# Optimization experiments

Measured on AMD Instinct MI355X. Metric: run time of the kernel, lower is better.

Reference implementation:

```python
import jax, jax.numpy as jnp
import numpy as np

B, S, I, C, N = 8, 50, 20, 64, 4096  # batch, max seq len, items per set, channels, num_items


def setup_inputs() -> dict:
    key = jax.random.key(0)
    k1, k2, k3, k4, k5 = jax.random.split(key, 5)
    input_tensor = jax.random.normal(k1, (B, S, I, C), dtype=jnp.float32)
    items_id = jax.random.randint(k2, (B, S, I), 0, N)
    # seq lengths in [1, S] (original truncates each user's sequence)
    batch_seq_length = jax.random.randint(k3, (B,), 1, S + 1)
    items_embedding = jax.random.normal(k4, (N, C), dtype=jnp.float32) * 0.02
    proj_w = jax.random.normal(k5, (C, C), dtype=jnp.float32) / jnp.sqrt(jnp.float32(C))
    proj_b = jnp.zeros((C,), dtype=jnp.float32)
    return {
        "input_tensor": input_tensor,
        "items_embedding": items_embedding,
        "proj_w": proj_w,
        "proj_b": proj_b,
        "items_id": items_id,
        "batch_seq_length": batch_seq_length,
    }


def reference(input_tensor, items_embedding, proj_w, proj_b, items_id, batch_seq_length):
    # Dropout layers are identity in eval mode.
    Bb, Ss, Ii, Cc = input_tensor.shape
    Nn = items_embedding.shape[0]

    # valid sequence positions per user: seq_index < batch_seq_length[b]
    seq_mask = (jnp.arange(Ss)[None, :] < batch_seq_length[:, None]).astype(input_tensor.dtype)  # [B,S]
    m = seq_mask[:, :, None]  # [B,S,1], all I item slots valid inside a valid position

    # segment-mean over item occurrences (replaces the Python dict-of-lists + stack/mean)
    flat_ids = (items_id + jnp.arange(Bb)[:, None, None] * Nn).reshape(-1)  # [B*S*I]
    data = (input_tensor * m[..., None]).reshape(-1, Cc)                    # [B*S*I, C]
    sums = jax.ops.segment_sum(data, flat_ids, num_segments=Bb * Nn).reshape(Bb, Nn, Cc)
    counts = jax.ops.segment_sum(jnp.broadcast_to(m, (Bb, Ss, Ii)).reshape(-1),
                                 flat_ids, num_segments=Bb * Nn).reshape(Bb, Nn)
    present = counts > 0                                                    # user's unique historical items
    mean = sums / jnp.maximum(counts, 1.0)[..., None]                       # [B,N,C]

    # attention of all items over the user's unique historical-item embeddings
    scores = jnp.einsum('nc,bmc->bnm', items_embedding, mean)               # [B,N,N]
    scores = jax.nn.leaky_relu(scores, negative_slope=0.2)
    scores = jnp.where(present[:, None, :], scores, jnp.float32(-1e30))     # softmax only over present items
    attn = jax.nn.softmax(scores, axis=-1)
    user_items_embedding = jnp.einsum('bnm,bmc->bnc', attn, mean)           # [B,N,C]

    proj = user_items_embedding @ proj_w.T + proj_b                         # Linear(C,C)
    return (proj * items_embedding[None]).sum(axis=-1)                      # [B,N]
```

## Files before the change

### kernel.cpp

```cpp
#include <hip/hip_runtime.h>

#define Bb 8
#define Ss 50
#define Ii 20
#define Cc 64
#define Nn 4096
#define MAXM 1024
#define POSB (Ss * Ii)

typedef unsigned short ushort_t;
typedef __attribute__((ext_vector_type(8))) short short8;
typedef __attribute__((ext_vector_type(4))) float f32x4;

__device__ inline ushort_t bf16_rn(float x) {
    unsigned u = __float_as_uint(x);
    u = u + 0x7FFFu + ((u >> 16) & 1u);
    return (ushort_t)(u >> 16);
}
__device__ inline float bf16_f(ushort_t h) { return __uint_as_float(((unsigned)h) << 16); }

__device__ inline short8 cvthi8(float4 a, float4 b) {
    short8 r;
    r[0] = (short)bf16_rn(a.x); r[1] = (short)bf16_rn(a.y);
    r[2] = (short)bf16_rn(a.z); r[3] = (short)bf16_rn(a.w);
    r[4] = (short)bf16_rn(b.x); r[5] = (short)bf16_rn(b.y);
    r[6] = (short)bf16_rn(b.z); r[7] = (short)bf16_rn(b.w);
    return r;
}
__device__ inline short8 cvtlo8(float4 a, float4 b, short8 hi) {
    short8 r;
    r[0] = (short)bf16_rn(a.x - bf16_f((ushort_t)hi[0]));
    r[1] = (short)bf16_rn(a.y - bf16_f((ushort_t)hi[1]));
    r[2] = (short)bf16_rn(a.z - bf16_f((ushort_t)hi[2]));
    r[3] = (short)bf16_rn(a.w - bf16_f((ushort_t)hi[3]));
    r[4] = (short)bf16_rn(b.x - bf16_f((ushort_t)hi[4]));
    r[5] = (short)bf16_rn(b.y - bf16_f((ushort_t)hi[5]));
    r[6] = (short)bf16_rn(b.z - bf16_f((ushort_t)hi[6]));
    r[7] = (short)bf16_rn(b.w - bf16_f((ushort_t)hi[7]));
    return r;
}

__global__ __launch_bounds__(1024) void aux_kernel(
    const float* __restrict__ input, const int* __restrict__ ids,
    const int* __restrict__ seqlen, const float* __restrict__ E,
    const float* __restrict__ W, const float* __restrict__ bias,
    int* __restrict__ Mcnt, int* __restrict__ slotHead, int* __restrict__ gnext,
    float* __restrict__ cvec, float* __restrict__ Fbuf) {
    __shared__ int smem[5120];
    int tid = threadIdx.x;

    if (blockIdx.x < Bb) {
        int b = blockIdx.x;
        int* head = smem;
        __shared__ int mcnt;
        for (int i = tid; i < Nn; i += 1024) head[i] = -1;
        if (tid == 0) mcnt = 0;
        __syncthreads();
        int P = seqlen[b] * Ii;
        if (tid < P) {
            int id = ids[b * POSB + tid];
            gnext[b * POSB + tid] = atomicExch(&head[id], tid);
        }
        __syncthreads();
        for (int i = tid; i < Nn; i += 1024) {
            int h = head[i];
            if (h >= 0) slotHead[b * MAXM + atomicAdd(&mcnt, 1)] = h;
        }
        __syncthreads();
        if (tid == 0) Mcnt[b] = mcnt;
    } else {
        int pb = blockIdx.x - Bb;
        float* wlds = (float*)smem;
        float* elds = (float*)smem + 4096;
        int n0 = pb * 16;
#pragma unroll
        for (int i = 0; i < 4; i++) wlds[tid + 1024 * i] = W[tid + 1024 * i];
        float ev = E[(size_t)n0 * Cc + tid];
        elds[tid] = ev;
        __syncthreads();
        int nl = tid >> 6, k = tid & 63;
        float acc = 0.f;
#pragma unroll
        for (int c = 0; c < Cc; c++) acc = fmaf(elds[nl * Cc + c], wlds[c * Cc + k], acc);
        Fbuf[(size_t)(n0 + nl) * Cc + k] = acc;
        float p = ev * bias[k];
#pragma unroll
        for (int off = 32; off; off >>= 1) p += __shfl_down(p, off);
        if (k == 0) cvec[n0 + nl] = p;
    }
}

__global__ __launch_bounds__(256) void mean_kernel(
    const float* __restrict__ input, const int* __restrict__ slotHead,
    const int* __restrict__ gnext, const int* __restrict__ Mcnt,
    ushort_t* __restrict__ Mhi) {
    int w = (blockIdx.x * 256 + threadIdx.x) >> 6;
    int lane = threadIdx.x & 63;
    int b = w >> 10;
    int slot = w & (MAXM - 1);
    if (slot >= Mcnt[b]) return;
    int p = slotHead[b * MAXM + slot];
    float sum = 0.f; int k = 0;
    while (p >= 0) {
        sum += input[((size_t)(b * POSB + p)) * Cc + lane];
        k++;
        p = gnext[b * POSB + p];
    }
    Mhi[((size_t)(b * MAXM + slot)) * Cc + lane] = bf16_rn(sum / (float)k);
}

#define MFMA(A, B, C) __builtin_amdgcn_mfma_f32_16x16x32_bf16(A, B, C, 0, 0, 0)

__global__ __launch_bounds__(512) void main_kernel(
    const float* __restrict__ E, const float* __restrict__ Fbuf,
    const ushort_t* __restrict__ Mhi,
    const int* __restrict__ Mcnt, const float* __restrict__ cvec,
    float* __restrict__ out) {
    __shared__ float part[2][64];
    int idx = blockIdx.x;
    int ntile = idx >> 3;
    int b = (idx + (idx >> 3) + (idx >> 8)) & 7;
    int tid = threadIdx.x;
    int wave = tid >> 6, lane = tid & 63;
    int wn = wave & 3, wm = wave >> 2;
    int kq = lane >> 4;
    int n = ntile * 64 + wn * 16 + (lane & 15);

    const float4* ep = (const float4*)(E + (size_t)n * Cc + kq * 8);
    const float4* fp = (const float4*)(Fbuf + (size_t)n * Cc + kq * 8);
    float4 ea = ep[0], eb = ep[1], ec = ep[8], ed = ep[9];
    float4 fa = fp[0], fb = fp[1], fc = fp[8], fd = fp[9];
    short8 Eh0 = cvthi8(ea, eb), Eh1 = cvthi8(ec, ed);
    short8 Fh0 = cvthi8(fa, fb), Fh1 = cvthi8(fc, fd);
    short8 Fl0 = cvtlo8(fa, fb, Fh0), Fl1 = cvtlo8(fc, fd, Fh1);

    int M = Mcnt[b];
    int nmt = (M + 15) >> 4;
    size_t ab = ((size_t)(b * MAXM) + (lane & 15)) * Cc + kq * 8;

    size_t a0 = ab + (size_t)wm * (16 * Cc);
    short8 Ah0 = *(const short8*)(Mhi + a0), Ah1 = *(const short8*)(Mhi + a0 + 32);

    float l = 0.f, av = 0.f;
    int rowg = kq * 4;

#pragma unroll 1
    for (int mt = wm; mt < nmt; mt += 2) {
        int mtn = (mt + 2 < nmt) ? mt + 2 : mt;
        size_t an = ab + (size_t)mtn * (16 * Cc);
        short8 Nh0 = *(const short8*)(Mhi + an), Nh1 = *(const short8*)(Mhi + an + 32);

        f32x4 S = {0.f, 0.f, 0.f, 0.f}, D = {0.f, 0.f, 0.f, 0.f};
        S = MFMA(Ah0, Eh0, S); S = MFMA(Ah1, Eh1, S);
        D = MFMA(Ah0, Fh0, D); D = MFMA(Ah1, Fh1, D);
        D = MFMA(Ah0, Fl0, D); D = MFMA(Ah1, Fl1, D);

        int mrow = mt * 16 + rowg;
#pragma unroll
        for (int r = 0; r < 4; r++) {
            float s = S[r];
            float sc = fmaxf(s, 0.2f * s);
            float ex = __expf(sc);
            ex = (mrow + r < M) ? ex : 0.f;
            l += ex;
            av = fmaf(ex, D[r], av);
        }
        Ah0 = Nh0; Ah1 = Nh1;
    }

#pragma unroll
    for (int mask = 16; mask <= 32; mask <<= 1) {
        l  += __shfl_xor(l,  mask);
        av += __shfl_xor(av, mask);
    }
    if (wm == 1 && lane < 16) {
        part[0][wn * 16 + lane] = l;
        part[1][wn * 16 + lane] = av;
    }
    __syncthreads();
    if (wm == 0 && lane < 16) {
        float lp  = part[0][wn * 16 + lane];
        float avp = part[1][wn * 16 + lane];
        out[b * Nn + n] = (av + avp) / (l + lp) + cvec[n];
    }
}

extern "C" void kernel_launch(void* const* d_in, const int* in_sizes, int n_in,
                              void* d_out, int out_size, void* d_ws, size_t ws_size,
                              hipStream_t stream) {
    (void)in_sizes; (void)n_in; (void)out_size; (void)ws_size;
    const float* input  = (const float*)d_in[0];
    const float* E      = (const float*)d_in[1];
    const float* W      = (const float*)d_in[2];
    const float* bias   = (const float*)d_in[3];
    const int*   ids    = (const int*)d_in[4];
    const int*   seqlen = (const int*)d_in[5];
    float* out = (float*)d_out;

    int*      Mcnt     = (int*)d_ws;
    int*      slotHead = Mcnt + 16;
    int*      gnext    = slotHead + Bb * MAXM;
    float*    cvec     = (float*)(gnext + Bb * POSB);
    float*    Fbuf     = cvec + Nn;
    ushort_t* Mhi      = (ushort_t*)(Fbuf + (size_t)Nn * Cc);

    aux_kernel <<<Bb + Nn / 16, 1024, 0, stream>>>(input, ids, seqlen, E, W, bias,
                                                   Mcnt, slotHead, gnext, cvec, Fbuf);
    mean_kernel<<<Bb * MAXM / 4, 256, 0, stream>>>(input, slotHead, gnext, Mcnt, Mhi);
    main_kernel<<<Bb * (Nn / 64), 512, 0, stream>>>(E, Fbuf, Mhi, Mcnt, cvec, out);
}
```

Measured before the change: 89.05 us.

## Fuse three kernels into one cooperative kernel with grid syncs

Replaces the aux, mean and main kernel launches with a single cooperative kernel of 512 blocks that separates the phases with grid.sync(). The goal is to remove launch overhead and the gaps between the three dependent kernels. The slot compaction now uses a wave ballot and prefix count instead of a per-thread shared atomic, and masked rows zero the D value before accumulating. The cost is that grid-wide barriers and a fixed grid size cap occupancy and parallelism in each phase. The old three-kernel path is kept as a fallback if the cooperative launch fails.

```diff
diff --git a/kernel.cpp b/kernel.cpp
--- a/kernel.cpp
+++ b/kernel.cpp
@@ -1,4 +1,7 @@
 #include <hip/hip_runtime.h>
+#include <hip/hip_cooperative_groups.h>
+
+namespace cg = cooperative_groups;
 
 #define Bb 8
 #define Ss 50
@@ -7,6 +10,7 @@
 #define Nn 4096
 #define MAXM 1024
 #define POSB (Ss * Ii)
+#define GRID 512
 
 typedef unsigned short ushort_t;
 typedef __attribute__((ext_vector_type(8))) short short8;
@@ -40,6 +44,166 @@
     return r;
 }
 
+#define MFMA(A, B, C) __builtin_amdgcn_mfma_f32_16x16x32_bf16(A, B, C, 0, 0, 0)
+
+__global__ __launch_bounds__(512, 4) void fused_kernel(
+    const float* __restrict__ input, const int* __restrict__ ids,
+    const int* __restrict__ seqlen, const float* __restrict__ E,
+    const float* __restrict__ W, const float* __restrict__ bias,
+    int* __restrict__ Mcnt, int* __restrict__ slotHead, int* __restrict__ gnext,
+    float* __restrict__ cvec, float* __restrict__ Fbuf,
+    ushort_t* __restrict__ Mhi, float* __restrict__ out) {
+    __shared__ int smem[4608];
+    __shared__ int mcnt;
+    cg::grid_group grid = cg::this_grid();
+    int tid = threadIdx.x;
+    int wave = tid >> 6, lane = tid & 63;
+
+    if (blockIdx.x < Bb) {
+        int b = blockIdx.x;
+        int* head = smem;
+        for (int i = tid; i < Nn; i += 512) head[i] = -1;
+        if (tid == 0) mcnt = 0;
+        __syncthreads();
+        int P = seqlen[b] * Ii;
+        for (int p = tid; p < P; p += 512)
+            gnext[b * POSB + p] = atomicExch(&head[ids[b * POSB + p]], p);
+        __syncthreads();
+        for (int i = tid; i < Nn; i += 512) {
+            int h = head[i];
+            unsigned long long m = __ballot(h >= 0);
+            int cnt = __popcll(m);
+            int base;
+            if (lane == 0) base = atomicAdd(&mcnt, cnt);
+            base = __shfl(base, 0);
+            if (h >= 0) {
+                int rank = __popcll(m & ((1ull << lane) - 1ull));
+                slotHead[b * MAXM + base + rank] = h;
+            }
+        }
+        __syncthreads();
+        if (tid == 0) Mcnt[b] = mcnt;
+        __syncthreads();
+    }
+
+    {
+        float* wlds = (float*)smem;
+        float* elds = (float*)smem + 4096;
+        int n0 = blockIdx.x * 8;
+#pragma unroll
+        for (int i = 0; i < 8; i++) wlds[tid + 512 * i] = W[tid + 512 * i];
+        int nl = wave, k = lane;
+        float ev = E[(size_t)(n0 + nl) * Cc + k];
+        elds[tid] = ev;
+        __syncthreads();
+        float acc = 0.f;
+#pragma unroll
+        for (int c = 0; c < Cc; c++) acc = fmaf(elds[nl * Cc + c], wlds[c * Cc + k], acc);
+        Fbuf[(size_t)(n0 + nl) * Cc + k] = acc;
+        float p = ev * bias[k];
+#pragma unroll
+        for (int off = 32; off; off >>= 1) p += __shfl_down(p, off);
+        if (k == 0) cvec[n0 + nl] = p;
+    }
+
+    __threadfence();
+    grid.sync();
+
+    {
+        int w = blockIdx.x * 8 + wave;
+        int b = w >> 9;
+        int s0 = (w & 511) * 2;
+        int M = Mcnt[b];
+#pragma unroll
+        for (int si = 0; si < 2; si++) {
+            int s = s0 + si;
+            if (s < M) {
+                int p = slotHead[b * MAXM + s];
+                float sum = 0.f; int k = 0;
+                while (p >= 0) {
+                    sum += input[((size_t)(b * POSB + p)) * Cc + lane];
+                    k++;
+                    p = gnext[b * POSB + p];
+                }
+                Mhi[((size_t)(b * MAXM + s)) * Cc + lane] = bf16_rn(sum / (float)k);
+            }
+        }
+    }
+
+    __threadfence();
+    grid.sync();
+
+    {
+        float* part = (float*)smem;
+        int idx = blockIdx.x;
+        int ntile = idx >> 3;
+        int b = (idx + (idx >> 3) + (idx >> 8)) & 7;
+        int wn = wave & 3, wm = wave >> 2;
+        int kq = lane >> 4;
+        int n = ntile * 64 + wn * 16 + (lane & 15);
+
+        const float4* ep = (const float4*)(E + (size_t)n * Cc + kq * 8);
+        const float4* fp = (const float4*)(Fbuf + (size_t)n * Cc + kq * 8);
+        float4 ea = ep[0], eb = ep[1], ec = ep[8], ed = ep[9];
+        float4 fa = fp[0], fb = fp[1], fc = fp[8], fd = fp[9];
+        short8 Eh0 = cvthi8(ea, eb), Eh1 = cvthi8(ec, ed);
+        short8 Fh0 = cvthi8(fa, fb), Fh1 = cvthi8(fc, fd);
+        short8 Fl0 = cvtlo8(fa, fb, Fh0), Fl1 = cvtlo8(fc, fd, Fh1);
+
+        int M = Mcnt[b];
+        int nmt = (M + 15) >> 4;
+        size_t ab = ((size_t)(b * MAXM) + (lane & 15)) * Cc + kq * 8;
+
+        size_t a0 = ab + (size_t)wm * (16 * Cc);
+        short8 Ah0 = *(const short8*)(Mhi + a0), Ah1 = *(const short8*)(Mhi + a0 + 32);
+
+        float l = 0.f, av = 0.f;
+        int rowg = kq * 4;
+
+#pragma unroll 1
+        for (int mt = wm; mt < nmt; mt += 2) {
+            int mtn = (mt + 2 < nmt) ? mt + 2 : mt;
+            size_t an = ab + (size_t)mtn * (16 * Cc);
+            short8 Nh0 = *(const short8*)(Mhi + an), Nh1 = *(const short8*)(Mhi + an + 32);
+
+            f32x4 S = {0.f, 0.f, 0.f, 0.f}, D = {0.f, 0.f, 0.f, 0.f};
+            S = MFMA(Ah0, Eh0, S); S = MFMA(Ah1, Eh1, S);
+            D = MFMA(Ah0, Fh0, D); D = MFMA(Ah1, Fh1, D);
+            D = MFMA(Ah0, Fl0, D); D = MFMA(Ah1, Fl1, D);
+
+            int mrow = mt * 16 + rowg;
+#pragma unroll
+            for (int r = 0; r < 4; r++) {
+                float s = S[r];
+                float sc = fmaxf(s, 0.2f * s);
+                float ex = __expf(sc);
+                bool ok = (mrow + r < M);
+                ex = ok ? ex : 0.f;
+                float df = ok ? D[r] : 0.f;
+                l += ex;
+                av = fmaf(ex, df, av);
+            }
+            Ah0 = Nh0; Ah1 = Nh1;
+        }
+
+#pragma unroll
+        for (int mask = 16; mask <= 32; mask <<= 1) {
+            l  += __shfl_xor(l,  mask);
+            av += __shfl_xor(av, mask);
+        }
+        if (wm == 1 && lane < 16) {
+            part[wn * 16 + lane]      = l;
+            part[64 + wn * 16 + lane] = av;
+        }
+        __syncthreads();
+        if (wm == 0 && lane < 16) {
+            float lp  = part[wn * 16 + lane];
+            float avp = part[64 + wn * 16 + lane];
+            out[b * Nn + n] = (av + avp) / (l + lp) + cvec[n];
+        }
+    }
+}
+
 __global__ __launch_bounds__(1024) void aux_kernel(
     const float* __restrict__ input, const int* __restrict__ ids,
     const int* __restrict__ seqlen, const float* __restrict__ E,
@@ -48,7 +212,6 @@
     float* __restrict__ cvec, float* __restrict__ Fbuf) {
     __shared__ int smem[5120];
     int tid = threadIdx.x;
-
     if (blockIdx.x < Bb) {
         int b = blockIdx.x;
         int* head = smem;
@@ -109,8 +272,6 @@
     Mhi[((size_t)(b * MAXM + slot)) * Cc + lane] = bf16_rn(sum / (float)k);
 }
 
-#define MFMA(A, B, C) __builtin_amdgcn_mfma_f32_16x16x32_bf16(A, B, C, 0, 0, 0)
-
 __global__ __launch_bounds__(512) void main_kernel(
     const float* __restrict__ E, const float* __restrict__ Fbuf,
     const ushort_t* __restrict__ Mhi,
@@ -125,7 +286,6 @@
     int wn = wave & 3, wm = wave >> 2;
     int kq = lane >> 4;
     int n = ntile * 64 + wn * 16 + (lane & 15);
-
     const float4* ep = (const float4*)(E + (size_t)n * Cc + kq * 8);
     const float4* fp = (const float4*)(Fbuf + (size_t)n * Cc + kq * 8);
     float4 ea = ep[0], eb = ep[1], ec = ep[8], ed = ep[9];
@@ -133,41 +293,36 @@
     short8 Eh0 = cvthi8(ea, eb), Eh1 = cvthi8(ec, ed);
     short8 Fh0 = cvthi8(fa, fb), Fh1 = cvthi8(fc, fd);
     short8 Fl0 = cvtlo8(fa, fb, Fh0), Fl1 = cvtlo8(fc, fd, Fh1);
-
     int M = Mcnt[b];
     int nmt = (M + 15) >> 4;
     size_t ab = ((size_t)(b * MAXM) + (lane & 15)) * Cc + kq * 8;
-
     size_t a0 = ab + (size_t)wm * (16 * Cc);
     short8 Ah0 = *(const short8*)(Mhi + a0), Ah1 = *(const short8*)(Mhi + a0 + 32);
-
     float l = 0.f, av = 0.f;
     int rowg = kq * 4;
-
 #pragma unroll 1
     for (int mt = wm; mt < nmt; mt += 2) {
         int mtn = (mt + 2 < nmt) ? mt + 2 : mt;
         size_t an = ab + (size_t)mtn * (16 * Cc);
         short8 Nh0 = *(const short8*)(Mhi + an), Nh1 = *(const short8*)(Mhi + an + 32);
-
         f32x4 S = {0.f, 0.f, 0.f, 0.f}, D = {0.f, 0.f, 0.f, 0.f};
         S = MFMA(Ah0, Eh0, S); S = MFMA(Ah1, Eh1, S);
         D = MFMA(Ah0, Fh0, D); D = MFMA(Ah1, Fh1, D);
         D = MFMA(Ah0, Fl0, D); D = MFMA(Ah1, Fl1, D);
-
         int mrow = mt * 16 + rowg;
 #pragma unroll
         for (int r = 0; r < 4; r++) {
             float s = S[r];
             float sc = fmaxf(s, 0.2f * s);
             float ex = __expf(sc);
-            ex = (mrow + r < M) ? ex : 0.f;
+            bool ok = (mrow + r < M);
+            ex = ok ? ex : 0.f;
+            float df = ok ? D[r] : 0.f;
             l += ex;
-            av = fmaf(ex, D[r], av);
+            av = fmaf(ex, df, av);
         }
         Ah0 = Nh0; Ah1 = Nh1;
     }
-
 #pragma unroll
     for (int mask = 16; mask <= 32; mask <<= 1) {
         l  += __shfl_xor(l,  mask);
@@ -204,8 +359,17 @@
     float*    Fbuf     = cvec + Nn;
     ushort_t* Mhi      = (ushort_t*)(Fbuf + (size_t)Nn * Cc);
 
-    aux_kernel <<<Bb + Nn / 16, 1024, 0, stream>>>(input, ids, seqlen, E, W, bias,
-                                                   Mcnt, slotHead, gnext, cvec, Fbuf);
-    mean_kernel<<<Bb * MAXM / 4, 256, 0, stream>>>(input, slotHead, gnext, Mcnt, Mhi);
-    main_kernel<<<Bb * (Nn / 64), 512, 0, stream>>>(E, Fbuf, Mhi, Mcnt, cvec, out);
-}
+    void* args[] = {(void*)&input, (void*)&ids, (void*)&seqlen, (void*)&E,
+                    (void*)&W, (void*)&bias, (void*)&Mcnt, (void*)&slotHead,
+                    (void*)&gnext, (void*)&cvec, (void*)&Fbuf, (void*)&Mhi,
+                    (void*)&out};
+    hipError_t err = hipLaunchCooperativeKernel(
+        reinterpret_cast<void*>(fused_kernel), dim3(GRID), dim3(512),
+        args, 0, stream);
+    if (err != hipSuccess) {
+        aux_kernel <<<Bb + Nn / 16, 1024, 0, stream>>>(input, ids, seqlen, E, W, bias,
+                                                       Mcnt, slotHead, gnext, cvec, Fbuf);
+        mean_kernel<<<Bb * MAXM / 4, 256, 0, stream>>>(input, slotHead, gnext, Mcnt, Mhi);
+        main_kernel<<<Bb * (Nn / 64), 512, 0, stream>>>(E, Fbuf, Mhi, Mcnt, cvec, out);
+    }
+}
```

Result: slower. 317.8 us (+256.9%).
